# Kernel optimization log

Measured on AMD Instinct MI355X. Metric: run time of the kernel, lower is better.

## Reference

```python
import jax, jax.numpy as jnp
import numpy as np

N_U, N_P, E, E_LAB = 100000, 50000, 2000000, 500000
D_U, D_P, H = 64, 128, 64


def _seg_mean(feat, idx, n):
    # scatter-mean: sum per destination / clamp(count, 1)
    s = jax.ops.segment_sum(feat, idx, num_segments=n)
    c = jax.ops.segment_sum(jnp.ones((idx.shape[0],), feat.dtype), idx, num_segments=n)
    return s / jnp.maximum(c, 1.0)[:, None]


def setup_inputs() -> dict:
    key = jax.random.key(0)
    ks = jax.random.split(key, 16)
    inp = {
        'x_user': jax.random.normal(ks[0], (N_U, D_U), jnp.float32),
        'x_product': jax.random.normal(ks[1], (N_P, D_P), jnp.float32),
        'W1_buys_l': jax.random.normal(ks[2], (D_U, H), jnp.float32) * 0.05,
        'b1_buys': jnp.zeros((H,), jnp.float32),
        'W1_buys_r': jax.random.normal(ks[3], (D_P, H), jnp.float32) * 0.05,
        'W1_rev_l': jax.random.normal(ks[4], (D_P, H), jnp.float32) * 0.05,
        'b1_rev': jnp.zeros((H,), jnp.float32),
        'W1_rev_r': jax.random.normal(ks[5], (D_U, H), jnp.float32) * 0.05,
        'W2_buys_l': jax.random.normal(ks[6], (H, H), jnp.float32) * 0.05,
        'b2_buys': jnp.zeros((H,), jnp.float32),
        'W2_buys_r': jax.random.normal(ks[7], (H, H), jnp.float32) * 0.05,
        'W2_rev_l': jax.random.normal(ks[8], (H, H), jnp.float32) * 0.05,
        'b2_rev': jnp.zeros((H,), jnp.float32),
        'W2_rev_r': jax.random.normal(ks[9], (H, H), jnp.float32) * 0.05,
        'edge_src': jax.random.randint(ks[10], (E,), 0, N_U, jnp.int32),
        'edge_dst': jax.random.randint(ks[11], (E,), 0, N_P, jnp.int32),
        'lab_u': jax.random.randint(ks[12], (E_LAB,), 0, N_U, jnp.int32),
        'lab_p': jax.random.randint(ks[13], (E_LAB,), 0, N_P, jnp.int32),
    }
    return inp


def reference(x_user, x_product, W1_buys_l, b1_buys, W1_buys_r, W1_rev_l, b1_rev, W1_rev_r,
              W2_buys_l, b2_buys, W2_buys_r, W2_rev_l, b2_rev, W2_rev_r,
              edge_src, edge_dst, lab_u, lab_p):
    # SAGEConv (mean aggr): out_dst = mean_agg(x_src) @ W_l + b + x_dst @ W_r
    def sage(x_src, x_dst, src, dst, n_dst, Wl, b, Wr):
        agg = _seg_mean(x_src[src], dst, n_dst)
        return agg @ Wl + b + x_dst @ Wr

    n_u, n_p = x_user.shape[0], x_product.shape[0]
    # layer 1 (per edge type, hetero) + relu
    h_p = jax.nn.relu(sage(x_user, x_product, edge_src, edge_dst, n_p, W1_buys_l, b1_buys, W1_buys_r))
    h_u = jax.nn.relu(sage(x_product, x_user, edge_dst, edge_src, n_u, W1_rev_l, b1_rev, W1_rev_r))
    # layer 2
    h_p2 = sage(h_u, h_p, edge_src, edge_dst, n_p, W2_buys_l, b2_buys, W2_buys_r)
    h_u2 = sage(h_p, h_u, edge_dst, edge_src, n_u, W2_rev_l, b2_rev, W2_rev_r)
    # classifier: per-label-edge dot product
    return jnp.sum(h_u2[lab_u] * h_p2[lab_p], axis=-1)
```

## Files before the change

kernel.cpp:

```cpp
#include <hip/hip_runtime.h>


using u16 = unsigned short;
using u32 = unsigned int;

__device__ __forceinline__ u16 bf16r(float f) {
    u32 b = __float_as_uint(f);
    b += 0x7fffu + ((b >> 16) & 1u);
    return (u16)(b >> 16);
}
__device__ __forceinline__ float bflo(u32 u) { return __uint_as_float(u << 16); }
__device__ __forceinline__ float bfhi(u32 u) { return __uint_as_float(u & 0xffff0000u); }

#define BSH 8
#define MAXB 512
#define CHUNK 4096
#define RPT 16
#define HB 512

__global__ __launch_bounds__(256) void k_histCast(const int* __restrict__ esrc,
                                                  const int* __restrict__ edst,
                                                  int* __restrict__ bcntP,
                                                  int* __restrict__ bcntU,
                                                  int NBP, int NBU, int E,
                                                  const float* __restrict__ xc,
                                                  u16* __restrict__ yc, int n8) {
    __shared__ int hP[MAXB];
    __shared__ int hU[MAXB];
    int tid = threadIdx.x;
    if ((int)blockIdx.x >= HB) {
        int i = (blockIdx.x - HB) * 256 + tid;
        if (i < n8) {
            const float4* x4 = (const float4*)xc;
            float4 a = x4[i * 2], b = x4[i * 2 + 1];
            uint4 o;
            o.x = (u32)bf16r(a.x) | ((u32)bf16r(a.y) << 16);
            o.y = (u32)bf16r(a.z) | ((u32)bf16r(a.w) << 16);
            o.z = (u32)bf16r(b.x) | ((u32)bf16r(b.y) << 16);
            o.w = (u32)bf16r(b.z) | ((u32)bf16r(b.w) << 16);
            ((uint4*)yc)[i] = o;
        }
        return;
    }
    for (int i = tid; i < MAXB; i += 256) { hP[i] = 0; hU[i] = 0; }
    __syncthreads();
    int E4 = E >> 2;
    const int4* s4 = (const int4*)esrc;
    const int4* d4 = (const int4*)edst;
    int stride = HB * 256;
    for (int i = blockIdx.x * 256 + tid; i < E4; i += stride) {
        int4 s = s4[i], d = d4[i];
        atomicAdd(&hU[s.x >> BSH], 1); atomicAdd(&hU[s.y >> BSH], 1);
        atomicAdd(&hU[s.z >> BSH], 1); atomicAdd(&hU[s.w >> BSH], 1);
        atomicAdd(&hP[d.x >> BSH], 1); atomicAdd(&hP[d.y >> BSH], 1);
        atomicAdd(&hP[d.z >> BSH], 1); atomicAdd(&hP[d.w >> BSH], 1);
    }
    if (blockIdx.x == 0 && tid < (E & 3)) {
        int e = E4 * 4 + tid;
        atomicAdd(&hU[esrc[e] >> BSH], 1);
        atomicAdd(&hP[edst[e] >> BSH], 1);
    }
    __syncthreads();
    for (int i = tid; i < NBP; i += 256) if (hP[i]) atomicAdd(&bcntP[i], hP[i]);
    for (int i = tid; i < NBU; i += 256) if (hU[i]) atomicAdd(&bcntU[i], hU[i]);
}

__global__ __launch_bounds__(256) void k_scanBuckets(const int* __restrict__ cntP,
                                                     int* __restrict__ basesP,
                                                     int* __restrict__ curP, int NBP,
                                                     const int* __restrict__ cntU,
                                                     int* __restrict__ basesU,
                                                     int* __restrict__ curU, int NBU) {
    const int* cnt; int* bases; int* cur; int NB;
    if (blockIdx.x == 0) { cnt = cntP; bases = basesP; cur = curP; NB = NBP; }
    else                 { cnt = cntU; bases = basesU; cur = curU; NB = NBU; }
    __shared__ int sA[MAXB];
    __shared__ int sB[MAXB];
    int tid = threadIdx.x;
    int v0 = (tid < NB) ? cnt[tid] : 0;
    int v1 = (tid + 256 < NB) ? cnt[tid + 256] : 0;
    sA[tid] = v0; sA[tid + 256] = v1;
    __syncthreads();
    int* src = sA; int* dst = sB;
    for (int off = 1; off < MAXB; off <<= 1) {
        dst[tid] = src[tid] + ((tid >= off) ? src[tid - off] : 0);
        int i2 = tid + 256;
        dst[i2] = src[i2] + ((i2 >= off) ? src[i2 - off] : 0);
        __syncthreads();
        int* t = src; src = dst; dst = t;
    }
    if (tid < NB)       { bases[tid] = src[tid] - v0;             cur[tid] = src[tid] - v0; }
    if (tid + 256 < NB) { bases[tid + 256] = src[tid + 256] - v1; cur[tid + 256] = src[tid + 256] - v1; }
    if (tid == 0) bases[NB] = src[MAXB - 1];
}

__global__ __launch_bounds__(256) void k_partition2(
    const int* __restrict__ keysP, const int* __restrict__ payP,
    int* __restrict__ curPp, uint2* __restrict__ pairsP, int NBP,
    const int* __restrict__ keysU, const int* __restrict__ payU,
    int* __restrict__ curUp, uint2* __restrict__ pairsU, int NBU,
    int E, int pblocks) {
    __shared__ int hist[MAXB];
    __shared__ int sA[MAXB];
    __shared__ int sB[MAXB];
    __shared__ int bx[MAXB];
    __shared__ int gbase[MAXB];
    __shared__ uint2 prs[CHUNK];
    const int* keys; const int* payload; int* cursor; uint2* pairs; int NB, cb;
    if ((int)blockIdx.x < pblocks) {
        keys = keysP; payload = payP; cursor = curPp; pairs = pairsP; NB = NBP;
        cb = blockIdx.x;
    } else {
        keys = keysU; payload = payU; cursor = curUp; pairs = pairsU; NB = NBU;
        cb = blockIdx.x - pblocks;
    }
    int tid = threadIdx.x;
    int i0 = cb * CHUNK;
    int count = min(CHUNK, E - i0);
    for (int i = tid; i < MAXB; i += 256) hist[i] = 0;
    __syncthreads();
    int keyr[RPT], payr[RPT], rankr[RPT];
#pragma unroll
    for (int r = 0; r < RPT; ++r) {
        int idx = r * 256 + tid;
        if (idx < count) {
            int k = keys[i0 + idx];
            keyr[r] = k;
            payr[r] = payload[i0 + idx];
            rankr[r] = atomicAdd(&hist[k >> BSH], 1);
        } else keyr[r] = -1;
    }
    __syncthreads();
    sA[tid] = hist[tid]; sA[tid + 256] = hist[tid + 256];
    __syncthreads();
    int* src = sA; int* dst = sB;
    for (int off = 1; off < MAXB; off <<= 1) {
        dst[tid] = src[tid] + ((tid >= off) ? src[tid - off] : 0);
        int i2 = tid + 256;
        dst[i2] = src[i2] + ((i2 >= off) ? src[i2 - off] : 0);
        __syncthreads();
        int* t = src; src = dst; dst = t;
    }
    bx[tid] = src[tid] - hist[tid];
    bx[tid + 256] = src[tid + 256] - hist[tid + 256];
    __syncthreads();
    for (int b = tid; b < NB; b += 256) {
        int c = hist[b];
        gbase[b] = c ? atomicAdd(&cursor[b], c) : 0;
    }
#pragma unroll
    for (int r = 0; r < RPT; ++r) {
        if (keyr[r] >= 0)
            prs[bx[keyr[r] >> BSH] + rankr[r]] = make_uint2((u32)keyr[r], (u32)payr[r]);
    }
    __syncthreads();
    for (int j = tid; j < count; j += 256) {
        uint2 pr = prs[j];
        int b = pr.x >> BSH;
        pairs[gbase[b] + (j - bx[b])] = pr;
    }
}

__global__ __launch_bounds__(256) void k_bucketFill(
    const uint2* __restrict__ pairsP, const int* __restrict__ basesP, int NBP,
    int* __restrict__ nbr_p, int* __restrict__ deg_p, int* __restrict__ ptr_p, int NP,
    const uint2* __restrict__ pairsU, const int* __restrict__ basesU, int NBU,
    int* __restrict__ nbr_u, int* __restrict__ deg_u, int* __restrict__ ptr_u, int NU) {
    const uint2* pairs; const int* bases; int* nbr; int* deg; int* ptr; int N; int bucket;
    if ((int)blockIdx.x < NBP) {
        pairs = pairsP; bases = basesP; nbr = nbr_p; deg = deg_p; ptr = ptr_p; N = NP;
        bucket = blockIdx.x;
    } else {
        pairs = pairsU; bases = basesU; nbr = nbr_u; deg = deg_u; ptr = ptr_u; N = NU;
        bucket = blockIdx.x - NBP;
    }
    int tid = threadIdx.x;
    int base = bases[bucket];
    int cnt = bases[bucket + 1] - base;
    __shared__ int h[256];
    __shared__ int s[256];
    __shared__ int cur[256];
    h[tid] = 0;
    __syncthreads();
    for (int j = tid; j < cnt; j += 256) atomicAdd(&h[pairs[base + j].x & 255], 1);
    __syncthreads();
    int d = h[tid];
    s[tid] = d;
    __syncthreads();
    for (int off = 1; off < 256; off <<= 1) {
        int v = (tid >= off) ? s[tid - off] : 0;
        __syncthreads();
        s[tid] += v;
        __syncthreads();
    }
    int excl = s[tid] - d;
    int node = bucket * 256 + tid;
    if (node < N) { deg[node] = d; ptr[node] = base + excl; }
    cur[tid] = excl;
    __syncthreads();
    for (int j = tid; j < cnt; j += 256) {
        uint2 pr = pairs[base + j];
        int pos = atomicAdd(&cur[pr.x & 255], 1);
        nbr[base + pos] = (int)(pr.y << 7);
    }
}

#define ACC8(A0,A1,A2,A3,A4,A5,A6,A7,V) \
    A0 += bflo((V).x); A1 += bfhi((V).x); A2 += bflo((V).y); A3 += bfhi((V).y); \
    A4 += bflo((V).z); A5 += bfhi((V).z); A6 += bflo((V).w); A7 += bfhi((V).w);

__global__ __launch_bounds__(256) void k_gather2(
    const u16* __restrict__ yA, const int* __restrict__ nbrA, const int* __restrict__ stpA,
    const int* __restrict__ degA, float* __restrict__ aggA, int NA,
    const u16* __restrict__ yB, const int* __restrict__ nbrB, const int* __restrict__ stpB,
    const int* __restrict__ degB, float* __restrict__ aggB, int NB) {
    int w = (blockIdx.x * 256 + threadIdx.x) >> 6;
    int lane = threadIdx.x & 63;
    if (w >= NA + NB) return;
    const u16* y; const int* nbr; const int* stp; const int* deg; float* agg; int n;
    if (w < NA) { y = yA; nbr = nbrA; stp = stpA; deg = degA; agg = aggA; n = w; }
    else        { y = yB; nbr = nbrB; stp = stpB; deg = degB; agg = aggB; n = w - NA; }
    const int q = lane >> 3, t = lane & 7;
    const int d = deg[n];
    const int st = stp[n];
    const char* yb = (const char*)y + t * 16;
    float a0=0,a1=0,a2=0,a3=0,a4=0,a5=0,a6=0,a7=0;
    for (int j = 0; j < d; j += 64) {
        const int cnt = min(d - j, 64);
        int offv = 0;
        if (lane < cnt) offv = nbr[st + j + lane];
#define GLD(R) \
        int g##R = __shfl(offv, R * 8 + q, 64); \
        uint4 v##R = make_uint4(0u, 0u, 0u, 0u); \
        if (R * 8 + q < cnt) v##R = *(const uint4*)(yb + g##R);
        GLD(0) GLD(1) GLD(2) GLD(3) GLD(4) GLD(5) GLD(6) GLD(7)
#undef GLD
#define ACCR(R) if (R * 8 < cnt) { ACC8(a0,a1,a2,a3,a4,a5,a6,a7,v##R) }
        ACCR(0) ACCR(1) ACCR(2) ACCR(3) ACCR(4) ACCR(5) ACCR(6) ACCR(7)
#undef ACCR
    }
#pragma unroll
    for (int m = 8; m < 64; m <<= 1) {
        a0 += __shfl_xor(a0, m, 64); a1 += __shfl_xor(a1, m, 64);
        a2 += __shfl_xor(a2, m, 64); a3 += __shfl_xor(a3, m, 64);
        a4 += __shfl_xor(a4, m, 64); a5 += __shfl_xor(a5, m, 64);
        a6 += __shfl_xor(a6, m, 64); a7 += __shfl_xor(a7, m, 64);
    }
    if (q == 0) {
        float dinv = 1.0f / (float)max(d, 1);
        float* dstp = agg + n * 64 + t * 8;
        *(float4*)dstp       = make_float4(a0 * dinv, a1 * dinv, a2 * dinv, a3 * dinv);
        *(float4*)(dstp + 4) = make_float4(a4 * dinv, a5 * dinv, a6 * dinv, a7 * dinv);
    }
}

#define FMA_ROW(ACC, O, W4) \
    ACC[0] += (O) * (W4).x; ACC[1] += (O) * (W4).y; \
    ACC[2] += (O) * (W4).z; ACC[3] += (O) * (W4).w;

template <int K, int ROWS, bool RELU, bool EMIT, bool PRE, bool BIAS, bool STORE>
__global__ __launch_bounds__(256) void k_ctile(const float* __restrict__ pre,
                                               const float* __restrict__ bias,
                                               const float* __restrict__ x,
                                               const float* __restrict__ W,
                                               float* __restrict__ h,
                                               u16* __restrict__ hbf, int N) {
    constexpr int RR = ROWS / 16;
    constexpr int STRIDE = K + 4;
    constexpr int KF4 = K / 4;
    __shared__ float Ws[K * 64];
    __shared__ float op[ROWS * STRIDE];
    const int tid = threadIdx.x;
    for (int i = tid; i < K * 16; i += 256)
        ((float4*)Ws)[i] = ((const float4*)W)[i];
    const int c4 = (tid & 15) * 4;
    const int rb = (tid >> 4) * RR;
    float bx_ = 0.f, by_ = 0.f, bz_ = 0.f, bw_ = 0.f;
    if (BIAS) {
        float4 b4 = *(const float4*)(bias + c4);
        bx_ = b4.x; by_ = b4.y; bz_ = b4.z; bw_ = b4.w;
    }
    const int ntiles = (N + ROWS - 1) / ROWS;
    for (int tile = blockIdx.x; tile < ntiles; tile += gridDim.x) {
        const int row0 = tile * ROWS;
        __syncthreads();
        for (int i = tid; i < ROWS * KF4; i += 256) {
            int r = i / KF4, k4 = (i % KF4) * 4;
            int row = row0 + r;
            float4 v = make_float4(0.f, 0.f, 0.f, 0.f);
            if (row < N) v = *(const float4*)(x + (size_t)row * K + k4);
            *(float4*)(op + r * STRIDE + k4) = v;
        }
        __syncthreads();
        float acc[RR][4];
#pragma unroll
        for (int i = 0; i < RR; ++i) {
            float px = 0.f, py = 0.f, pz = 0.f, pw = 0.f;
            if (PRE) {
                int row = row0 + rb + i;
                if (row < N) {
                    float4 p = *(const float4*)(pre + row * 64 + c4);
                    px = p.x; py = p.y; pz = p.z; pw = p.w;
                }
            }
            acc[i][0] = bx_ + px; acc[i][1] = by_ + py;
            acc[i][2] = bz_ + pz; acc[i][3] = bw_ + pw;
        }
        for (int kk = 0; kk < K; kk += 4) {
            float4 w0 = *(const float4*)(Ws + (kk + 0) * 64 + c4);
            float4 w1 = *(const float4*)(Ws + (kk + 1) * 64 + c4);
            float4 w2 = *(const float4*)(Ws + (kk + 2) * 64 + c4);
            float4 w3 = *(const float4*)(Ws + (kk + 3) * 64 + c4);
#pragma unroll
            for (int i = 0; i < RR; ++i) {
                float4 o = *(const float4*)(op + (rb + i) * STRIDE + kk);
                FMA_ROW(acc[i], o.x, w0);
                FMA_ROW(acc[i], o.y, w1);
                FMA_ROW(acc[i], o.z, w2);
                FMA_ROW(acc[i], o.w, w3);
            }
        }
#pragma unroll
        for (int i = 0; i < RR; ++i) {
            int row = row0 + rb + i;
            if (row >= N) continue;
            float v0 = acc[i][0], v1 = acc[i][1], v2 = acc[i][2], v3 = acc[i][3];
            if (RELU) {
                v0 = fmaxf(v0, 0.f); v1 = fmaxf(v1, 0.f);
                v2 = fmaxf(v2, 0.f); v3 = fmaxf(v3, 0.f);
            }
            if (STORE)
                *(float4*)(h + row * 64 + c4) = make_float4(v0, v1, v2, v3);
            if (EMIT) {
                uint2 o;
                o.x = (u32)bf16r(v0) | ((u32)bf16r(v1) << 16);
                o.y = (u32)bf16r(v2) | ((u32)bf16r(v3) << 16);
                *(uint2*)(hbf + row * 64 + c4) = o;
            }
        }
    }
}

template <bool PRE, bool BIAS>
__global__ __launch_bounds__(256) void k_ctilePair64(
    const float* __restrict__ pre0, const float* __restrict__ bias0,
    const float* __restrict__ x0, const float* __restrict__ W0,
    float* __restrict__ h0, int N0, int g0,
    const float* __restrict__ pre1, const float* __restrict__ bias1,
    const float* __restrict__ x1, const float* __restrict__ W1,
    float* __restrict__ h1, int N1) {
    constexpr int ROWS = 64, RR = 4, STRIDE = 68, KF4 = 16;
    __shared__ float Ws[64 * 64];
    __shared__ float op[ROWS * STRIDE];
    const float* pre; const float* bias; const float* x; const float* W; float* h;
    int N, bid, gsz;
    if ((int)blockIdx.x < g0) {
        pre = pre0; bias = bias0; x = x0; W = W0; h = h0; N = N0;
        bid = blockIdx.x; gsz = g0;
    } else {
        pre = pre1; bias = bias1; x = x1; W = W1; h = h1; N = N1;
        bid = blockIdx.x - g0; gsz = gridDim.x - g0;
    }
    const int tid = threadIdx.x;
    for (int i = tid; i < 64 * 16; i += 256)
        ((float4*)Ws)[i] = ((const float4*)W)[i];
    const int c4 = (tid & 15) * 4;
    const int rb = (tid >> 4) * RR;
    float bx_ = 0.f, by_ = 0.f, bz_ = 0.f, bw_ = 0.f;
    if (BIAS) {
        float4 b4 = *(const float4*)(bias + c4);
        bx_ = b4.x; by_ = b4.y; bz_ = b4.z; bw_ = b4.w;
    }
    const int ntiles = (N + ROWS - 1) / ROWS;
    for (int tile = bid; tile < ntiles; tile += gsz) {
        const int row0 = tile * ROWS;
        __syncthreads();
        for (int i = tid; i < ROWS * KF4; i += 256) {
            int r = i / KF4, k4 = (i % KF4) * 4;
            int row = row0 + r;
            float4 v = make_float4(0.f, 0.f, 0.f, 0.f);
            if (row < N) v = *(const float4*)(x + (size_t)row * 64 + k4);
            *(float4*)(op + r * STRIDE + k4) = v;
        }
        __syncthreads();
        float acc[RR][4];
#pragma unroll
        for (int i = 0; i < RR; ++i) {
            float px = 0.f, py = 0.f, pz = 0.f, pw = 0.f;
            if (PRE) {
                int row = row0 + rb + i;
                if (row < N) {
                    float4 p = *(const float4*)(pre + row * 64 + c4);
                    px = p.x; py = p.y; pz = p.z; pw = p.w;
                }
            }
            acc[i][0] = bx_ + px; acc[i][1] = by_ + py;
            acc[i][2] = bz_ + pz; acc[i][3] = bw_ + pw;
        }
        for (int kk = 0; kk < 64; kk += 4) {
            float4 w0 = *(const float4*)(Ws + (kk + 0) * 64 + c4);
            float4 w1 = *(const float4*)(Ws + (kk + 1) * 64 + c4);
            float4 w2 = *(const float4*)(Ws + (kk + 2) * 64 + c4);
            float4 w3 = *(const float4*)(Ws + (kk + 3) * 64 + c4);
#pragma unroll
            for (int i = 0; i < RR; ++i) {
                float4 o = *(const float4*)(op + (rb + i) * STRIDE + kk);
                FMA_ROW(acc[i], o.x, w0);
                FMA_ROW(acc[i], o.y, w1);
                FMA_ROW(acc[i], o.z, w2);
                FMA_ROW(acc[i], o.w, w3);
            }
        }
#pragma unroll
        for (int i = 0; i < RR; ++i) {
            int row = row0 + rb + i;
            if (row >= N) continue;
            *(float4*)(h + row * 64 + c4) =
                make_float4(acc[i][0], acc[i][1], acc[i][2], acc[i][3]);
        }
    }
}

__global__ __launch_bounds__(256) void k_classify4(const float* __restrict__ hu,
                                                   const float* __restrict__ hp,
                                                   const int* __restrict__ lu,
                                                   const int* __restrict__ lp,
                                                   float* __restrict__ out, int EL) {
    int w = (blockIdx.x * 256 + threadIdx.x) >> 6;
    int lane = threadIdx.x & 63;
    int q = lane >> 4, t = lane & 15;
    int e = w * 4 + q;
    float v = 0.f;
    if (e < EL) {
        int u = lu[e], p = lp[e];
        float4 a = *(const float4*)(hu + u * 64 + t * 4);
        float4 b = *(const float4*)(hp + p * 64 + t * 4);
        v = a.x * b.x + a.y * b.y + a.z * b.z + a.w * b.w;
    }
#pragma unroll
    for (int m = 1; m < 16; m <<= 1) v += __shfl_xor(v, m, 64);
    if (t == 0 && e < EL) out[e] = v;
}

extern "C" void kernel_launch(void* const* d_in, const int* in_sizes, int n_in,
                              void* d_out, int out_size, void* d_ws, size_t ws_size,
                              hipStream_t stream) {
    const float* x_user    = (const float*)d_in[0];
    const float* x_product = (const float*)d_in[1];
    const float* W1bl = (const float*)d_in[2];
    const float* b1b  = (const float*)d_in[3];
    const float* W1br = (const float*)d_in[4];
    const float* W1rl = (const float*)d_in[5];
    const float* b1r  = (const float*)d_in[6];
    const float* W1rr = (const float*)d_in[7];
    const float* W2bl = (const float*)d_in[8];
    const float* b2b  = (const float*)d_in[9];
    const float* W2br = (const float*)d_in[10];
    const float* W2rl = (const float*)d_in[11];
    const float* b2r  = (const float*)d_in[12];
    const float* W2rr = (const float*)d_in[13];
    const int* esrc = (const int*)d_in[14];
    const int* edst = (const int*)d_in[15];
    const int* lu   = (const int*)d_in[16];
    const int* lp   = (const int*)d_in[17];

    const int NU = in_sizes[0] / 64;
    const int NP = in_sizes[1] / 128;
    const int E  = in_sizes[14];
    const int EL = in_sizes[16];
    const int NBP = (NP + 255) >> BSH;
    const int NBU = (NU + 255) >> BSH;

    char* ws = (char*)d_ws;
    size_t off = 0;
    auto alloc = [&](size_t bytes) -> void* {
        void* p = ws + off;
        off += (bytes + 255) & ~(size_t)255;
        return p;
    };
    int*   deg_u  = (int*)alloc((size_t)NU * 4);
    int*   deg_p  = (int*)alloc((size_t)NP * 4);
    int*   ptr_u  = (int*)alloc((size_t)NU * 4);
    int*   ptr_p  = (int*)alloc((size_t)NP * 4);
    int*   bcntP  = (int*)alloc((size_t)MAXB * 4);
    int*   bcntU  = (int*)alloc((size_t)MAXB * 4);
    int*   basesP = (int*)alloc((size_t)(MAXB + 1) * 4);
    int*   basesU = (int*)alloc((size_t)(MAXB + 1) * 4);
    int*   curP   = (int*)alloc((size_t)MAXB * 4);
    int*   curU   = (int*)alloc((size_t)MAXB * 4);
    int*   nbr_u  = (int*)alloc((size_t)E * 4);
    int*   nbr_p  = (int*)alloc((size_t)E * 4);
    size_t aggBytes = (size_t)(NP + NU) * 64 * 4;
    size_t pairBytes = (size_t)E * 8 * 2;
    char* uni = (char*)alloc(aggBytes > pairBytes ? aggBytes : pairBytes);
    float* aggP   = (float*)uni;
    float* aggU   = (float*)(uni + (size_t)NP * 64 * 4);
    uint2* pairsP = (uint2*)uni;
    uint2* pairsU = (uint2*)(uni + (size_t)E * 8);
    u16*   bfA    = (u16*)alloc((size_t)NU * 64 * 2);
    u16*   bfB    = (u16*)alloc((size_t)NP * 64 * 2);
    float* h_p    = (float*)alloc((size_t)NP * 64 * 4);
    float* h_u    = (float*)alloc((size_t)NU * 64 * 4);

    hipMemsetAsync(bcntP, 0, (size_t)MAXB * 2 * 4, stream);
    const int n8 = NU * 64 / 8;
    const int castBlocks = (n8 + 255) / 256;
    k_histCast<<<HB + castBlocks, 256, 0, stream>>>(esrc, edst, bcntP, bcntU, NBP, NBU, E,
                                                    x_user, bfA, n8);
    k_scanBuckets<<<2, 256, 0, stream>>>(bcntP, basesP, curP, NBP, bcntU, basesU, curU, NBU);
    const int pblocks = (E + CHUNK - 1) / CHUNK;
    k_partition2<<<2 * pblocks, 256, 0, stream>>>(edst, esrc, curP, pairsP, NBP,
                                                  esrc, edst, curU, pairsU, NBU, E, pblocks);
    k_bucketFill<<<NBP + NBU, 256, 0, stream>>>(pairsP, basesP, NBP, nbr_p, deg_p, ptr_p, NP,
                                                pairsU, basesU, NBU, nbr_u, deg_u, ptr_u, NU);

    {
        const int tiles = (NP + 31) / 32;
        k_ctile<128, 32, false, true, false, false, false><<<(tiles < 768 ? tiles : 768), 256, 0, stream>>>(
            nullptr, nullptr, x_product, W1rl, nullptr, bfB, NP);
    }

    const int tP64 = (NP + 63) / 64, tP32 = (NP + 31) / 32;
    const int tU64 = (NU + 63) / 64;
    auto cap = [](int t, int c) { return t < c ? t : c; };
    const int gP = cap(tP64, 512), gU = cap(tU64, 512);

    k_gather2<<<(NP + NU + 3) / 4, 256, 0, stream>>>(bfA, nbr_p, ptr_p, deg_p, aggP, NP,
                                                     bfB, nbr_u, ptr_u, deg_u, aggU, NU);
    k_ctile<64, 64, false, false, false, true, true><<<cap(tP64, 1024), 256, 0, stream>>>(
        nullptr, b1b, aggP, W1bl, h_p, nullptr, NP);
    k_ctile<128, 32, true, true, true, false, true><<<cap(tP32, 768), 256, 0, stream>>>(
        h_p, nullptr, x_product, W1br, h_p, bfB, NP);
    k_ctile<64, 64, true, true, true, true, true><<<cap(tU64, 1024), 256, 0, stream>>>(
        aggU, b1r, x_user, W1rr, h_u, bfA, NU);

    k_gather2<<<(NP + NU + 3) / 4, 256, 0, stream>>>(bfA, nbr_p, ptr_p, deg_p, aggP, NP,
                                                     bfB, nbr_u, ptr_u, deg_u, aggU, NU);
    k_ctilePair64<false, true><<<gP + gU, 256, 0, stream>>>(
        nullptr, b2b, aggP, W2bl, aggP, NP, gP,
        nullptr, b2r, aggU, W2rl, aggU, NU);
    k_ctilePair64<true, false><<<gP + gU, 256, 0, stream>>>(
        aggP, nullptr, h_p, W2br, h_p, NP, gP,
        aggU, nullptr, h_u, W2rr, h_u, NU);

    k_classify4<<<((EL + 3) / 4 + 3) / 4, 256, 0, stream>>>(h_u, h_p, lu, lp, (float*)d_out, EL);
}
```

Before: 519.3 us.

## Fuse per-type SAGE linear layers into paired and concatenated-K tile kernels

Layer 1's root transform x_product@W1br is now computed before the first gather, so it no longer sits after it. The product-side neighbour transform and the user-side transform then run together in one paired kernel that adds the precomputed term and applies ReLU with a bf16 emit. Layer 2's two separate paired launches become one concatenated-K (128) kernel that reads agg and h together against stacked weights, which drops the intermediate write and re-read of agg and one launch. The cost is larger shared-memory tiles with fewer rows per tile, and an in-place write of h_p/h_u in the concat kernel that depends on each tile reading its rows before writing them.

```diff
diff --git a/kernel.cpp b/kernel.cpp
--- a/kernel.cpp
+++ b/kernel.cpp
@@ -341,24 +341,25 @@
     }
 }
 
-template <bool PRE, bool BIAS>
-__global__ __launch_bounds__(256) void k_ctilePair64(
+template <bool PRE, bool BIAS, bool RELU, bool EMIT>
+__global__ __launch_bounds__(256) void k_ctilePair64X(
     const float* __restrict__ pre0, const float* __restrict__ bias0,
     const float* __restrict__ x0, const float* __restrict__ W0,
-    float* __restrict__ h0, int N0, int g0,
+    float* __restrict__ h0, u16* __restrict__ hbf0, int N0, int g0,
     const float* __restrict__ pre1, const float* __restrict__ bias1,
     const float* __restrict__ x1, const float* __restrict__ W1,
-    float* __restrict__ h1, int N1) {
+    float* __restrict__ h1, u16* __restrict__ hbf1, int N1) {
     constexpr int ROWS = 64, RR = 4, STRIDE = 68, KF4 = 16;
     __shared__ float Ws[64 * 64];
     __shared__ float op[ROWS * STRIDE];
-    const float* pre; const float* bias; const float* x; const float* W; float* h;
+    const float* pre; const float* bias; const float* x; const float* W;
+    float* h; u16* hbf;
     int N, bid, gsz;
     if ((int)blockIdx.x < g0) {
-        pre = pre0; bias = bias0; x = x0; W = W0; h = h0; N = N0;
+        pre = pre0; bias = bias0; x = x0; W = W0; h = h0; hbf = hbf0; N = N0;
         bid = blockIdx.x; gsz = g0;
     } else {
-        pre = pre1; bias = bias1; x = x1; W = W1; h = h1; N = N1;
+        pre = pre1; bias = bias1; x = x1; W = W1; h = h1; hbf = hbf1; N = N1;
         bid = blockIdx.x - g0; gsz = gridDim.x - g0;
     }
     const int tid = threadIdx.x;
@@ -398,6 +399,92 @@
             acc[i][2] = bz_ + pz; acc[i][3] = bw_ + pw;
         }
         for (int kk = 0; kk < 64; kk += 4) {
+            float4 w0 = *(const float4*)(Ws + (kk + 0) * 64 + c4);
+            float4 w1 = *(const float4*)(Ws + (kk + 1) * 64 + c4);
+            float4 w2 = *(const float4*)(Ws + (kk + 2) * 64 + c4);
+            float4 w3 = *(const float4*)(Ws + (kk + 3) * 64 + c4);
+#pragma unroll
+            for (int i = 0; i < RR; ++i) {
+                float4 o = *(const float4*)(op + (rb + i) * STRIDE + kk);
+                FMA_ROW(acc[i], o.x, w0);
+                FMA_ROW(acc[i], o.y, w1);
+                FMA_ROW(acc[i], o.z, w2);
+                FMA_ROW(acc[i], o.w, w3);
+            }
+        }
+#pragma unroll
+        for (int i = 0; i < RR; ++i) {
+            int row = row0 + rb + i;
+            if (row >= N) continue;
+            float v0 = acc[i][0], v1 = acc[i][1], v2 = acc[i][2], v3 = acc[i][3];
+            if (RELU) {
+                v0 = fmaxf(v0, 0.f); v1 = fmaxf(v1, 0.f);
+                v2 = fmaxf(v2, 0.f); v3 = fmaxf(v3, 0.f);
+            }
+            *(float4*)(h + row * 64 + c4) = make_float4(v0, v1, v2, v3);
+            if (EMIT) {
+                uint2 o;
+                o.x = (u32)bf16r(v0) | ((u32)bf16r(v1) << 16);
+                o.y = (u32)bf16r(v2) | ((u32)bf16r(v3) << 16);
+                *(uint2*)(hbf + row * 64 + c4) = o;
+            }
+        }
+    }
+}
+
+template <bool BIAS>
+__global__ __launch_bounds__(256) void k_ctilePairCat(
+    const float* __restrict__ bias0, const float* __restrict__ xa0,
+    const float* __restrict__ xb0, const float* __restrict__ Wa0,
+    const float* __restrict__ Wb0, float* __restrict__ h0, int N0, int g0,
+    const float* __restrict__ bias1, const float* __restrict__ xa1,
+    const float* __restrict__ xb1, const float* __restrict__ Wa1,
+    const float* __restrict__ Wb1, float* __restrict__ h1, int N1) {
+    constexpr int ROWS = 32, RR = 2, STRIDE = 132, KF4 = 32;
+    __shared__ float Ws[128 * 64];
+    __shared__ float op[ROWS * STRIDE];
+    const float* bias; const float* xa; const float* xb;
+    const float* Wa; const float* Wb; float* h;
+    int N, bid, gsz;
+    if ((int)blockIdx.x < g0) {
+        bias = bias0; xa = xa0; xb = xb0; Wa = Wa0; Wb = Wb0; h = h0; N = N0;
+        bid = blockIdx.x; gsz = g0;
+    } else {
+        bias = bias1; xa = xa1; xb = xb1; Wa = Wa1; Wb = Wb1; h = h1; N = N1;
+        bid = blockIdx.x - g0; gsz = gridDim.x - g0;
+    }
+    const int tid = threadIdx.x;
+    for (int i = tid; i < 64 * 16; i += 256) {
+        ((float4*)Ws)[i]           = ((const float4*)Wa)[i];
+        ((float4*)Ws)[64 * 16 + i] = ((const float4*)Wb)[i];
+    }
+    const int c4 = (tid & 15) * 4;
+    const int rb = (tid >> 4) * RR;
+    float bx_ = 0.f, by_ = 0.f, bz_ = 0.f, bw_ = 0.f;
+    if (BIAS) {
+        float4 b4 = *(const float4*)(bias + c4);
+        bx_ = b4.x; by_ = b4.y; bz_ = b4.z; bw_ = b4.w;
+    }
+    const int ntiles = (N + ROWS - 1) / ROWS;
+    for (int tile = bid; tile < ntiles; tile += gsz) {
+        const int row0 = tile * ROWS;
+        __syncthreads();
+        for (int i = tid; i < ROWS * KF4; i += 256) {
+            int r = i >> 5, k4 = (i & 31) * 4;
+            int row = row0 + r;
+            float4 v = make_float4(0.f, 0.f, 0.f, 0.f);
+            if (row < N)
+                v = (k4 < 64) ? *(const float4*)(xa + (size_t)row * 64 + k4)
+                              : *(const float4*)(xb + (size_t)row * 64 + (k4 - 64));
+            *(float4*)(op + r * STRIDE + k4) = v;
+        }
+        __syncthreads();
+        float acc[RR][4];
+#pragma unroll
+        for (int i = 0; i < RR; ++i) {
+            acc[i][0] = bx_; acc[i][1] = by_; acc[i][2] = bz_; acc[i][3] = bw_;
+        }
+        for (int kk = 0; kk < 128; kk += 4) {
             float4 w0 = *(const float4*)(Ws + (kk + 0) * 64 + c4);
             float4 w1 = *(const float4*)(Ws + (kk + 1) * 64 + c4);
             float4 w2 = *(const float4*)(Ws + (kk + 2) * 64 + c4);
@@ -514,34 +601,33 @@
     k_bucketFill<<<NBP + NBU, 256, 0, stream>>>(pairsP, basesP, NBP, nbr_p, deg_p, ptr_p, NP,
                                                 pairsU, basesU, NBU, nbr_u, deg_u, ptr_u, NU);
 
-    {
-        const int tiles = (NP + 31) / 32;
-        k_ctile<128, 32, false, true, false, false, false><<<(tiles < 768 ? tiles : 768), 256, 0, stream>>>(
-            nullptr, nullptr, x_product, W1rl, nullptr, bfB, NP);
-    }
-
-    const int tP64 = (NP + 63) / 64, tP32 = (NP + 31) / 32;
-    const int tU64 = (NU + 63) / 64;
+    const int tP32 = (NP + 31) / 32;
+    const int tP64 = (NP + 63) / 64, tU64 = (NU + 63) / 64;
+    const int tU32 = (NU + 31) / 32;
     auto cap = [](int t, int c) { return t < c ? t : c; };
-    const int gP = cap(tP64, 512), gU = cap(tU64, 512);
+
+    k_ctile<128, 32, false, true, false, false, false><<<cap(tP32, 768), 256, 0, stream>>>(
+        nullptr, nullptr, x_product, W1rl, nullptr, bfB, NP);
+    k_ctile<128, 32, false, false, false, false, true><<<cap(tP32, 768), 256, 0, stream>>>(
+        nullptr, nullptr, x_product, W1br, h_p, nullptr, NP);
 
     k_gather2<<<(NP + NU + 3) / 4, 256, 0, stream>>>(bfA, nbr_p, ptr_p, deg_p, aggP, NP,
                                                      bfB, nbr_u, ptr_u, deg_u, aggU, NU);
-    k_ctile<64, 64, false, false, false, true, true><<<cap(tP64, 1024), 256, 0, stream>>>(
-        nullptr, b1b, aggP, W1bl, h_p, nullptr, NP);
-    k_ctile<128, 32, true, true, true, false, true><<<cap(tP32, 768), 256, 0, stream>>>(
-        h_p, nullptr, x_product, W1br, h_p, bfB, NP);
-    k_ctile<64, 64, true, true, true, true, true><<<cap(tU64, 1024), 256, 0, stream>>>(
-        aggU, b1r, x_user, W1rr, h_u, bfA, NU);
+    {
+        const int gP = cap(tP64, 512), gU = cap(tU64, 1024);
+        k_ctilePair64X<true, true, true, true><<<gP + gU, 256, 0, stream>>>(
+            h_p, b1b, aggP, W1bl, h_p, bfB, NP, gP,
+            aggU, b1r, x_user, W1rr, h_u, bfA, NU);
+    }
 
     k_gather2<<<(NP + NU + 3) / 4, 256, 0, stream>>>(bfA, nbr_p, ptr_p, deg_p, aggP, NP,
                                                      bfB, nbr_u, ptr_u, deg_u, aggU, NU);
-    k_ctilePair64<false, true><<<gP + gU, 256, 0, stream>>>(
-        nullptr, b2b, aggP, W2bl, aggP, NP, gP,
-        nullptr, b2r, aggU, W2rl, aggU, NU);
-    k_ctilePair64<true, false><<<gP + gU, 256, 0, stream>>>(
-        aggP, nullptr, h_p, W2br, h_p, NP, gP,
-        aggU, nullptr, h_u, W2rr, h_u, NU);
+    {
+        const int gP = cap(tP32, 512), gU = cap(tU32, 1024);
+        k_ctilePairCat<true><<<gP + gU, 256, 0, stream>>>(
+            b2b, aggP, h_p, W2bl, W2br, h_p, NP, gP,
+            b2r, aggU, h_u, W2rl, W2rr, h_u, NU);
+    }
 
     k_classify4<<<((EL + 3) / 4 + 3) / 4, 256, 0, stream>>>(h_u, h_p, lu, lp, (float*)d_out, EL);
 }
```

Result: faster. 497.6 us (-4.2%).
